# Optimization experiments

Measured on AMD Instinct MI355X. Metric: run time of the kernel, lower is better.

The kernel has to match this reference:

```python
import jax, jax.numpy as jnp
import numpy as np

B = 256      # graphs per batch
N_PER = 256  # nodes per graph
DEG = 16     # avg degree
F_IN = 128   # num_feats
H = 128      # nhid
C = 10       # num_classes
RATIO = 0.5
N = B * N_PER
E = B * N_PER * DEG
K1 = int(np.ceil(RATIO * N_PER))   # 128
K2 = int(np.ceil(RATIO * K1))      # 64
K3 = int(np.ceil(RATIO * K2))      # 32


def setup_inputs() -> dict:
    key = jax.random.key(0)
    ks = jax.random.split(key, 24)
    off = (jnp.arange(B, dtype=jnp.int32) * N_PER)[:, None]
    # random intra-graph edges (block-diagonal adjacency)
    src = (jax.random.randint(ks[0], (B, N_PER * DEG), 0, N_PER, dtype=jnp.int32) + off).reshape(-1)
    dst = (jax.random.randint(ks[1], (B, N_PER * DEG), 0, N_PER, dtype=jnp.int32) + off).reshape(-1)
    x = jax.random.normal(ks[2], (N, F_IN), jnp.float32)

    def glorot(k, fi, fo):
        s = jnp.sqrt(2.0 / (fi + fo)).astype(jnp.float32)
        return jax.random.normal(k, (fi, fo), jnp.float32) * s

    inp = dict(x=x, src=src, dst=dst)
    # GCN conv layers
    inp['W1'] = glorot(ks[3], F_IN, H); inp['b1'] = jnp.zeros((H,), jnp.float32)
    inp['W2'] = glorot(ks[4], H, H);    inp['b2'] = jnp.zeros((H,), jnp.float32)
    inp['W3'] = glorot(ks[5], H, H);    inp['b3'] = jnp.zeros((H,), jnp.float32)
    # SAGPool score layers (GCNConv(nhid, 1))
    inp['Ws1'] = glorot(ks[6], H, 1); inp['bs1'] = jnp.zeros((1,), jnp.float32)
    inp['Ws2'] = glorot(ks[7], H, 1); inp['bs2'] = jnp.zeros((1,), jnp.float32)
    inp['Ws3'] = glorot(ks[8], H, 1); inp['bs3'] = jnp.zeros((1,), jnp.float32)
    # MLP head
    inp['Wl1'] = glorot(ks[9], 2 * H, H);      inp['bl1'] = jnp.zeros((H,), jnp.float32)
    inp['Wl2'] = glorot(ks[10], H, H // 2);    inp['bl2'] = jnp.zeros((H // 2,), jnp.float32)
    inp['Wl3'] = glorot(ks[11], H // 2, C);    inp['bl3'] = jnp.zeros((C,), jnp.float32)
    return inp


def _gcn(x, W, b, src, dst, mask):
    # PyG GCNConv: add self-loops, sym-normalize by deg^-1/2, aggregate x@W.
    # `mask` marks surviving nodes; edges with a dropped endpoint are inactive,
    # which is equivalent to PyG's filter_adj subgraph relabeling.
    emf = (mask[src] & mask[dst]).astype(x.dtype)           # [E]
    deg = jax.ops.segment_sum(emf, dst, num_segments=N) + mask.astype(x.dtype)  # +1 self loop
    dinv = jnp.where(deg > 0, jax.lax.rsqrt(deg), 0.0)
    h = x @ W                                                # [N, out]
    w = emf * dinv[src] * dinv[dst]                          # [E]
    agg = jax.ops.segment_sum(h[src] * w[:, None], dst, num_segments=N)
    agg = agg + h * (dinv * dinv * mask.astype(x.dtype))[:, None]  # self-loop term
    return agg + b


def _sagpool(x, Ws, bs, src, dst, mask, k):
    # score = GCNConv(in,1)(x); keep top-k per graph; x = x[perm]*tanh(score[perm])
    score = _gcn(x, Ws, bs, src, dst, mask)[:, 0]            # [N]
    s = jnp.where(mask, score, -jnp.inf).reshape(B, N_PER)
    idx = jax.lax.top_k(s, k)[1]                             # [B, k]
    nm = jnp.zeros((B, N_PER), bool).at[jnp.arange(B)[:, None], idx].set(True).reshape(-1)
    x = x * jnp.tanh(score)[:, None] * nm[:, None].astype(x.dtype)
    return x, nm


def _readout(x, mask, count):
    # global_max_pool || global_mean_pool over surviving nodes of each graph
    xb = x.reshape(B, N_PER, H)
    mb = mask.reshape(B, N_PER)[:, :, None]
    mx = jnp.max(jnp.where(mb, xb, -jnp.inf), axis=1)
    mn = jnp.sum(xb * mb.astype(x.dtype), axis=1) / jnp.asarray(count, x.dtype)
    return jnp.concatenate([mx, mn], axis=1)                 # [B, 2H]


def reference(x, src, dst, W1, b1, W2, b2, W3, b3, Ws1, bs1, Ws2, bs2, Ws3, bs3,
              Wl1, bl1, Wl2, bl2, Wl3, bl3):
    m0 = jnp.ones((N,), bool)
    h = jax.nn.relu(_gcn(x, W1, b1, src, dst, m0))
    h, m1 = _sagpool(h, Ws1, bs1, src, dst, m0, K1)
    r1 = _readout(h, m1, K1)
    h = jax.nn.relu(_gcn(h, W2, b2, src, dst, m1))
    h, m2 = _sagpool(h, Ws2, bs2, src, dst, m1, K2)
    r2 = _readout(h, m2, K2)
    h = jax.nn.relu(_gcn(h, W3, b3, src, dst, m2))
    h, m3 = _sagpool(h, Ws3, bs3, src, dst, m2, K3)
    r3 = _readout(h, m3, K3)
    z = r1 + r2 + r3                                         # [B, 2H]
    z = jax.nn.relu(z @ Wl1 + bl1)
    # dropout skipped (eval mode / training=False)
    z = jax.nn.relu(z @ Wl2 + bl2)
    return jax.nn.log_softmax(jax.nn.relu(z @ Wl3 + bl3), axis=-1)
```

## Files before the change

### kernel.cpp

```cpp
#include <hip/hip_runtime.h>
#include <math.h>

#define NGRAPH 256
#define NPG 256
#define HF 128
#define EPG 4096
#define EPG2 4352
#define FSTR 132
#define PSTR 136

typedef __attribute__((ext_vector_type(8))) short bf16x8;
typedef __attribute__((ext_vector_type(4))) float f32x4;

template<int N> struct IC { static constexpr int value = N; };
template<bool B> struct BC { static constexpr bool value = B; };

static __device__ __forceinline__ unsigned bcu(float f){ return __builtin_bit_cast(unsigned, f); }
static __device__ __forceinline__ float bcf(unsigned u){ return __builtin_bit_cast(float, u); }
static __device__ __forceinline__ unsigned rtn16(float f){
  unsigned u = bcu(f);
  return (u + 0x7FFFu + ((u >> 16) & 1u)) >> 16;
}

__global__ __launch_bounds__(256) void prep_wt(const float* __restrict__ W1,
                                               const float* __restrict__ W2,
                                               const float* __restrict__ W3,
                                               short* __restrict__ Wt) {
  int idx = blockIdx.x * 256 + threadIdx.x;
  int L = idx >> 14, r = idx & 16383;
  int k = r >> 7, n = r & 127;
  const float* W = (L == 0) ? W1 : (L == 1) ? W2 : W3;
  float w = W[k*128 + n];
  unsigned hi = rtn16(w);
  float lo = w - bcf(hi << 16);
  short* Whi = Wt + (size_t)L * 2 * 16384;
  short* Wlo = Whi + 16384;
  Whi[n*128 + k] = (short)hi;
  Wlo[n*128 + k] = (short)(bcu(lo) >> 16);
}

#define BSTEP(OK, OI, KKc, Jc) do { \
  bool iLess = ((tid & (Jc)) == 0); \
  bool descR = ((tid & (KKc)) == 0); \
  bool myFirst = (kf > (OK)) || (kf == (OK) && ki < (OI)); \
  bool keep = (iLess == descR) ? myFirst : !myFirst; \
  if (!keep) { kf = (OK); ki = (OI); } \
} while (0)

#define WAVE0_SCAN() do { \
  if (wid == 0) { \
    int b4 = lane*4; \
    int c0=cntA[b4+0], c1=cntA[b4+1], c2=cntA[b4+2], c3=cntA[b4+3]; \
    int tot = c0+c1+c2+c3; \
    int run = tot; \
    _Pragma("unroll") \
    for (int off=1; off<64; off<<=1) { \
      int u = __shfl_up(run, off); \
      run += (lane >= off) ? u : 0; \
    } \
    int st = run - tot; \
    rloc[b4+0]=(unsigned short)st; \
    rloc[b4+1]=(unsigned short)(st+c0); \
    rloc[b4+2]=(unsigned short)(st+c0+c1); \
    rloc[b4+3]=(unsigned short)(st+c0+c1+c2); \
    curA[b4+0]=st; curA[b4+1]=st+c0; curA[b4+2]=st+c0+c1; curA[b4+3]=st+c0+c1+c2; \
    if (lane == 63) rloc[NPG] = (unsigned short)run; \
  } \
} while (0)

__global__ __launch_bounds__(1024, 4)
void fused_net(
    const float* __restrict__ x,
    const int* __restrict__ srcI, const int* __restrict__ dstI,
    const short* __restrict__ WtAll,
    const float* __restrict__ b1, const float* __restrict__ Ws1, const float* __restrict__ bs1,
    const float* __restrict__ b2, const float* __restrict__ Ws2, const float* __restrict__ bs2,
    const float* __restrict__ b3, const float* __restrict__ Ws3, const float* __restrict__ bs3,
    const float* __restrict__ Wl1, const float* __restrict__ bl1,
    const float* __restrict__ Wl2, const float* __restrict__ bl2,
    const float* __restrict__ Wl3, const float* __restrict__ bl3,
    float* __restrict__ out)
{
  __shared__ __align__(16) short hpair[2][NPG*PSTR];
  __shared__ unsigned char colS[EPG2 + 8];
  __shared__ unsigned short rloc[NPG+2];
  __shared__ unsigned selM[8];
  __shared__ float dinv[NPG];
  __shared__ __align__(16) float bvec[HF];
  __shared__ __align__(16) float wsv[HF];
  __shared__ float score[NPG];
  __shared__ float tscale[NPG];
  __shared__ float skey[NPG];
  __shared__ int   sidx[NPG];
  __shared__ unsigned char rank8[NPG];
  __shared__ unsigned char lut[NPG];
  __shared__ __align__(16) float red[1024];
  __shared__ float zacc[2*HF];

  float* tbufF = (float*)&hpair[0][0];
  short* hp0 = &hpair[0][0];
  short* hp1 = &hpair[1][0];
  int* cntA = (int*)skey;
  int* curA = sidx;

  int tid = threadIdx.x;
  int g = blockIdx.x;
  size_t nbase = (size_t)g * NPG;
  int lane = tid & 63, wid = tid >> 6;

  const float4* X4 = (const float4*)(x + nbase*HF);
  #pragma unroll
  for (int i = 0; i < 8; ++i) {
    int f4 = tid + i*1024;
    int r = f4 >> 5, kq = f4 & 31;
    float4 val = X4[f4];
    unsigned rx = rtn16(val.x), ry = rtn16(val.y), rz = rtn16(val.z), rw = rtn16(val.w);
    uint2 ph; ph.x = rx | (ry << 16); ph.y = rz | (rw << 16);
    float lx = val.x - bcf(rx << 16), ly = val.y - bcf(ry << 16);
    float lz = val.z - bcf(rz << 16), lw = val.w - bcf(rw << 16);
    uint2 pl; pl.x = (bcu(lx) >> 16) | (bcu(ly) & 0xFFFF0000u);
    pl.y = (bcu(lz) >> 16) | (bcu(lw) & 0xFFFF0000u);
    *(uint2*)&hp0[r*PSTR + kq*4] = ph;
    *(uint2*)&hp1[r*PSTR + kq*4] = pl;
  }

  int nb = g * NPG;
  int dloc[4], sloc[4];
  #pragma unroll
  for (int it = 0; it < 4; ++it) {
    int e = g*EPG + tid + it*1024;
    dloc[it] = dstI[e] - nb;
    sloc[it] = srcI[e] - nb;
  }

  if (tid < NPG) { cntA[tid] = 1; lut[tid] = (unsigned char)tid; }
  __syncthreads();
  #pragma unroll
  for (int it = 0; it < 4; ++it) atomicAdd(&cntA[dloc[it]], 1);
  __syncthreads();
  WAVE0_SCAN();
  __syncthreads();
  #pragma unroll
  for (int it = 0; it < 4; ++it) {
    int slot = atomicAdd(&curA[dloc[it]], 1);
    colS[slot] = (unsigned char)sloc[it];
  }
  if (tid < NPG) colS[rloc[tid+1] - 1] = (unsigned char)tid;

  auto run_layer = [&](auto nrc, auto kc, auto firstc, auto packc,
                       const short* Whi, const short* Wlo,
                       const float* bias, const float* Wsc, const float* bscp) {
    constexpr int NR = decltype(nrc)::value;
    constexpr int K  = decltype(kc)::value;
    constexpr bool FIRST = decltype(firstc)::value;
    constexpr bool PACK  = decltype(packc)::value;
    constexpr int TPN = 1024 / NR;
    constexpr int NI  = 32 / TPN;
    constexpr int SH  = (TPN == 4) ? 2 : ((TPN == 8) ? 3 : 4);
    int v = tid >> SH, q = tid & (TPN - 1);
    int cb0 = 4 * q;

    __syncthreads();

    if (tid < HF) { bvec[tid] = bias[tid]; wsv[tid] = Wsc[tid]; }
    if (tid < NR) dinv[tid] = 1.0f / sqrtf((float)((int)rloc[tid+1] - (int)rloc[tid]));

    {
      int rg = wid & 7, cg = wid >> 3;
      bool act = (rg * 32 < NR);
      int lr = lane & 15, lk8 = (lane >> 4) * 8;
      f32x4 tacc[2][4] = {};
      if (act) {
        #pragma unroll
        for (int kc2 = 0; kc2 < 4; ++kc2) {
          int k0 = kc2*32 + lk8;
          bf16x8 ah[2], al[2];
          #pragma unroll
          for (int rt = 0; rt < 2; ++rt) {
            int row = rg*32 + rt*16 + lr;
            ah[rt] = *(const bf16x8*)&hp0[row*PSTR + k0];
            al[rt] = *(const bf16x8*)&hp1[row*PSTR + k0];
          }
          #pragma unroll
          for (int ct = 0; ct < 4; ++ct) {
            int n = cg*64 + ct*16 + lr;
            bf16x8 bh = *(const bf16x8*)&Whi[n*HF + k0];
            bf16x8 bl = *(const bf16x8*)&Wlo[n*HF + k0];
            #pragma unroll
            for (int rt = 0; rt < 2; ++rt) {
              tacc[rt][ct] = __builtin_amdgcn_mfma_f32_16x16x32_bf16(ah[rt], bh, tacc[rt][ct], 0, 0, 0);
              tacc[rt][ct] = __builtin_amdgcn_mfma_f32_16x16x32_bf16(al[rt], bh, tacc[rt][ct], 0, 0, 0);
              tacc[rt][ct] = __builtin_amdgcn_mfma_f32_16x16x32_bf16(ah[rt], bl, tacc[rt][ct], 0, 0, 0);
            }
          }
        }
      }
      __syncthreads();
      if (act) {
        #pragma unroll
        for (int rt = 0; rt < 2; ++rt) {
          int row0 = rg*32 + rt*16 + (lane >> 4)*4;
          float d0 = dinv[row0+0], d1 = dinv[row0+1], d2 = dinv[row0+2], d3 = dinv[row0+3];
          #pragma unroll
          for (int ct = 0; ct < 4; ++ct) {
            int c = cg*64 + ct*16 + (lane & 15);
            tbufF[(row0+0)*FSTR + c] = tacc[rt][ct][0] * d0;
            tbufF[(row0+1)*FSTR + c] = tacc[rt][ct][1] * d1;
            tbufF[(row0+2)*FSTR + c] = tacc[rt][ct][2] * d2;
            tbufF[(row0+3)*FSTR + c] = tacc[rt][ct][3] * d3;
          }
        }
      }
    }
    __syncthreads();

    float4 hv[NI];
    {
      float4 acc[NI];
      #pragma unroll
      for (int j = 0; j < NI; ++j) { acc[j].x = acc[j].y = acc[j].z = acc[j].w = 0.f; }
      int e0 = rloc[v], e1 = rloc[v+1];
      int e = e0;
      for (; e + 1 < e1; e += 2) {
        int s0 = colS[e], s1 = colS[e+1];
        const float* g0 = &tbufF[s0*FSTR + cb0];
        const float* g1 = &tbufF[s1*FSTR + cb0];
        #pragma unroll
        for (int j = 0; j < NI; ++j) {
          float4 t0 = *(const float4*)&g0[j*4*TPN];
          float4 t1 = *(const float4*)&g1[j*4*TPN];
          acc[j].x += t0.x + t1.x; acc[j].y += t0.y + t1.y;
          acc[j].z += t0.z + t1.z; acc[j].w += t0.w + t1.w;
        }
      }
      if (e < e1) {
        const float* g0 = &tbufF[(int)colS[e]*FSTR + cb0];
        #pragma unroll
        for (int j = 0; j < NI; ++j) {
          float4 t0 = *(const float4*)&g0[j*4*TPN];
          acc[j].x += t0.x; acc[j].y += t0.y; acc[j].z += t0.z; acc[j].w += t0.w;
        }
      }
      float dv = dinv[v];
      float p = 0.f;
      #pragma unroll
      for (int j = 0; j < NI; ++j) {
        int ci = cb0 + j*4*TPN;
        float4 bv = *(const float4*)&bvec[ci];
        float4 wv = *(const float4*)&wsv[ci];
        float4 a;
        a.x = fmaxf(fmaf(dv, acc[j].x, bv.x), 0.f);
        a.y = fmaxf(fmaf(dv, acc[j].y, bv.y), 0.f);
        a.z = fmaxf(fmaf(dv, acc[j].z, bv.z), 0.f);
        a.w = fmaxf(fmaf(dv, acc[j].w, bv.w), 0.f);
        hv[j] = a;
        p += a.x*wv.x + a.y*wv.y + a.z*wv.z + a.w*wv.w;
      }
      red[tid] = p;
    }
    __syncthreads();
    if (tid < NR) {
      float s4 = 0.f;
      #pragma unroll
      for (int t = 0; t < TPN/4; ++t) {
        float4 qd = *(const float4*)&red[tid*TPN + 4*t];
        s4 += (qd.x + qd.y) + (qd.z + qd.w);
      }
      tscale[tid] = s4 * dinv[tid];
    }
    __syncthreads();
    if (tid < NR) {
      int e0 = rloc[tid], e1 = rloc[tid+1];
      float sa = 0.f;
      for (int e = e0; e < e1; ++e) sa += tscale[colS[e]];
      score[tid] = dinv[tid] * sa + bscp[0];
    }
    __syncthreads();

    float kf = -INFINITY; int ki = tid;
    if (tid < NR) {
      kf = score[tid];
      for (int kk = 2; kk <= 64; kk <<= 1)
        for (int j = kk >> 1; j > 0; j >>= 1) {
          float ok = __shfl_xor(kf, j);
          int   oi = __shfl_xor(ki, j);
          BSTEP(ok, oi, kk, j);
        }
    } else if (tid < NR + 8) selM[tid - NR] = 0u;

    if constexpr (NR == 256) {
      if (tid < NR) { skey[tid] = kf; sidx[tid] = ki; }
      __syncthreads();
      if (tid < NR) {
        int l = tid ^ 64; float ok = skey[l]; int oi = sidx[l];
        BSTEP(ok, oi, 128, 64);
        for (int j = 32; j > 0; j >>= 1) {
          float sk = __shfl_xor(kf, j); int si = __shfl_xor(ki, j);
          BSTEP(sk, si, 128, j);
        }
      }
      __syncthreads();
      if (tid < NR) { skey[tid] = kf; sidx[tid] = ki; }
      __syncthreads();
      if (tid < NR) {
        int l = tid ^ 128; float ok = skey[l]; int oi = sidx[l];
        BSTEP(ok, oi, 256, 128);
      }
      __syncthreads();
      if (tid < NR) { skey[tid] = kf; sidx[tid] = ki; }
      __syncthreads();
      if (tid < NR) {
        int l = tid ^ 64; float ok = skey[l]; int oi = sidx[l];
        BSTEP(ok, oi, 256, 64);
        for (int j = 32; j > 0; j >>= 1) {
          float sk = __shfl_xor(kf, j); int si = __shfl_xor(ki, j);
          BSTEP(sk, si, 256, j);
        }
      }
    } else if constexpr (NR == 128) {
      if (tid < NR) { skey[tid] = kf; sidx[tid] = ki; }
      __syncthreads();
      if (tid < NR) {
        int l = tid ^ 64; float ok = skey[l]; int oi = sidx[l];
        BSTEP(ok, oi, 128, 64);
        for (int j = 32; j > 0; j >>= 1) {
          float sk = __shfl_xor(kf, j); int si = __shfl_xor(ki, j);
          BSTEP(sk, si, 128, j);
        }
      }
    }
    if constexpr (NR == 64) __syncthreads();
    if constexpr (NR != 64 && NR != 256) __syncthreads();
    if (tid < K) atomicOr(&selM[ki >> 5], 1u << (ki & 31));
    __syncthreads();

    if (tid < NR) {
      unsigned wsel = selM[tid >> 5];
      bool sel = (wsel >> (tid & 31)) & 1;
      int r = __popc(wsel & ((1u << (tid & 31)) - 1u));
      for (int w = 0; w < (tid >> 5); ++w) r += __popc(selM[w]);
      rank8[tid] = sel ? (unsigned char)r : (unsigned char)0xFF;
      tscale[tid] = sel ? tanhf(score[tid]) : 0.f;
    }
    __syncthreads();
    if (tid < NPG) {
      int lv = lut[tid];
      lut[tid] = (lv < NR) ? rank8[lv] : (unsigned char)0xFF;
    }

    int rk = rank8[v];
    {
      float ts = tscale[v];
      if (rk != 0xFF) {
        #pragma unroll
        for (int j = 0; j < NI; ++j) {
          hv[j].x *= ts; hv[j].y *= ts; hv[j].z *= ts; hv[j].w *= ts;
          *(float4*)&tbufF[rk*FSTR + cb0 + j*4*TPN] = hv[j];
        }
      }
    }
    __syncthreads();

    {
      constexpr int RPG = K / 8;
      int f = tid & 127, vg = tid >> 7;
      float mx = -INFINITY, sm = 0.f;
      #pragma unroll
      for (int vr = 0; vr < RPG; ++vr) {
        float val = tbufF[(vg*RPG + vr)*FSTR + f];
        mx = fmaxf(mx, val); sm += val;
      }
      red[vg*HF + f] = mx;
      __syncthreads();
      if (tid < HF) {
        float zm = red[tid];
        #pragma unroll
        for (int q2 = 1; q2 < 8; ++q2) zm = fmaxf(zm, red[q2*HF + tid]);
        if (FIRST) zacc[tid] = zm; else zacc[tid] += zm;
      }
      __syncthreads();
      red[vg*HF + f] = sm;
      __syncthreads();
      if (tid < HF) {
        float zs = red[tid];
        #pragma unroll
        for (int q2 = 1; q2 < 8; ++q2) zs += red[q2*HF + tid];
        float mn = zs / (float)K;
        if (FIRST) zacc[HF + tid] = mn; else zacc[HF + tid] += mn;
      }
      __syncthreads();
    }

    if constexpr (PACK) {
      if (rk != 0xFF) {
        #pragma unroll
        for (int j = 0; j < NI; ++j) {
          int ci = cb0 + j*4*TPN;
          float4 val = hv[j];
          unsigned rx = rtn16(val.x), ry = rtn16(val.y), rz = rtn16(val.z), rw = rtn16(val.w);
          uint2 ph; ph.x = rx | (ry << 16); ph.y = rz | (rw << 16);
          float lx = val.x - bcf(rx << 16), ly = val.y - bcf(ry << 16);
          float lz = val.z - bcf(rz << 16), lw = val.w - bcf(rw << 16);
          uint2 pl; pl.x = (bcu(lx) >> 16) | (bcu(ly) & 0xFFFF0000u);
          pl.y = (bcu(lz) >> 16) | (bcu(lw) & 0xFFFF0000u);
          *(uint2*)&hp0[rk*PSTR + ci] = ph;
          *(uint2*)&hp1[rk*PSTR + ci] = pl;
        }
      }

      if (tid < K) cntA[tid] = 1; else if (tid < NPG) cntA[tid] = 0;
      __syncthreads();
      #pragma unroll
      for (int it = 0; it < 4; ++it) {
        int d2 = lut[dloc[it]], s2 = lut[sloc[it]];
        if (d2 < K && s2 < K) atomicAdd(&cntA[d2], 1);
      }
      __syncthreads();
      WAVE0_SCAN();
      __syncthreads();
      #pragma unroll
      for (int it = 0; it < 4; ++it) {
        int d2 = lut[dloc[it]], s2 = lut[sloc[it]];
        if (d2 < K && s2 < K) {
          int slot = atomicAdd(&curA[d2], 1);
          colS[slot] = (unsigned char)s2;
        }
      }
      if (tid < K) colS[rloc[tid+1] - 1] = (unsigned char)tid;
    }
  };

  run_layer(IC<256>{}, IC<128>{}, BC<true>{},  BC<true>{},
            WtAll,         WtAll + 16384, b1, Ws1, bs1);
  run_layer(IC<128>{}, IC<64>{},  BC<false>{}, BC<true>{},
            WtAll + 32768, WtAll + 49152, b2, Ws2, bs2);
  run_layer(IC<64>{},  IC<32>{},  BC<false>{}, BC<false>{},
            WtAll + 65536, WtAll + 81920, b3, Ws3, bs3);

  __syncthreads();

  {
    int o = tid & 127, kg = tid >> 7;
    float p = 0.f;
    int k0 = kg*32;
    for (int k = k0; k < k0+32; ++k) p += zacc[k]*Wl1[k*HF + o];
    red[kg*HF + o] = p;
    __syncthreads();
    if (tid < HF) {
      float a = bl1[tid];
      #pragma unroll
      for (int q2 = 0; q2 < 8; ++q2) a += red[q2*HF + tid];
      score[tid] = fmaxf(a, 0.f);
    }
    __syncthreads();
    if (tid < 512) {
      int o2 = tid & 63, kg2 = tid >> 6;
      float p2 = 0.f;
      int k0b = kg2*16;
      for (int k = k0b; k < k0b+16; ++k) p2 += score[k]*Wl2[k*64 + o2];
      red[kg2*64 + o2] = p2;
    }
    __syncthreads();
    if (tid < 64) {
      float a = bl2[tid];
      #pragma unroll
      for (int q2 = 0; q2 < 8; ++q2) a += red[q2*64 + tid];
      tscale[tid] = fmaxf(a, 0.f);
    }
    __syncthreads();
    if (tid < 10) {
      float a = bl3[tid];
      for (int k = 0; k < 64; ++k) a += tscale[k]*Wl3[k*10 + tid];
      dinv[tid] = fmaxf(a, 0.f);
    }
    __syncthreads();
    if (tid == 0) {
      float m = dinv[0];
      for (int i = 1; i < 10; ++i) m = fmaxf(m, dinv[i]);
      float s = 0.f;
      for (int i = 0; i < 10; ++i) s += expf(dinv[i] - m);
      red[0] = m; red[1] = logf(s);
    }
    __syncthreads();
    if (tid < 10) out[(size_t)g*10 + tid] = dinv[tid] - red[0] - red[1];
  }
}

extern "C" void kernel_launch(void* const* d_in, const int* in_sizes, int n_in,
                              void* d_out, int out_size, void* d_ws, size_t ws_size,
                              hipStream_t stream) {
  const float* x   = (const float*)d_in[0];
  const int*  srcI = (const int*)d_in[1];
  const int*  dstI = (const int*)d_in[2];
  const float* W1  = (const float*)d_in[3];
  const float* b1  = (const float*)d_in[4];
  const float* W2  = (const float*)d_in[5];
  const float* b2  = (const float*)d_in[6];
  const float* W3  = (const float*)d_in[7];
  const float* b3  = (const float*)d_in[8];
  const float* Ws1 = (const float*)d_in[9];
  const float* bs1 = (const float*)d_in[10];
  const float* Ws2 = (const float*)d_in[11];
  const float* bs2 = (const float*)d_in[12];
  const float* Ws3 = (const float*)d_in[13];
  const float* bs3 = (const float*)d_in[14];
  const float* Wl1 = (const float*)d_in[15];
  const float* bl1 = (const float*)d_in[16];
  const float* Wl2 = (const float*)d_in[17];
  const float* bl2 = (const float*)d_in[18];
  const float* Wl3 = (const float*)d_in[19];
  const float* bl3 = (const float*)d_in[20];
  float* out = (float*)d_out;

  short* WtAll = (short*)d_ws;

  prep_wt<<<192, 256, 0, stream>>>(W1, W2, W3, WtAll);
  fused_net<<<NGRAPH, 1024, 0, stream>>>(x, srcI, dstI, WtAll,
                                         b1, Ws1, bs1, b2, Ws2, bs2, b3, Ws3, bs3,
                                         Wl1, bl1, Wl2, bl2, Wl3, bl3, out);
}
```

Before: 93.69 us.

## Rebalance MFMA tiling across all waves, prefetch neighbor indices, merge readout reductions

```diff
diff --git a/kernel.cpp b/kernel.cpp
--- a/kernel.cpp
+++ b/kernel.cpp
@@ -95,6 +95,7 @@
   __shared__ unsigned char rank8[NPG];
   __shared__ unsigned char lut[NPG];
   __shared__ __align__(16) float red[1024];
+  __shared__ __align__(16) float red2[1024];
   __shared__ float zacc[2*HF];
 
   float* tbufF = (float*)&hpair[0][0];
@@ -157,6 +158,7 @@
     constexpr int TPN = 1024 / NR;
     constexpr int NI  = 32 / TPN;
     constexpr int SH  = (TPN == 4) ? 2 : ((TPN == 8) ? 3 : 4);
+    constexpr int RT  = NR / 64;
     int v = tid >> SH, q = tid & (TPN - 1);
     int cb0 = 4 * q;
 
@@ -166,49 +168,44 @@
     if (tid < NR) dinv[tid] = 1.0f / sqrtf((float)((int)rloc[tid+1] - (int)rloc[tid]));
 
     {
-      int rg = wid & 7, cg = wid >> 3;
-      bool act = (rg * 32 < NR);
+      int rg = wid & 3, cg = wid >> 2;
       int lr = lane & 15, lk8 = (lane >> 4) * 8;
-      f32x4 tacc[2][4] = {};
-      if (act) {
-        #pragma unroll
-        for (int kc2 = 0; kc2 < 4; ++kc2) {
-          int k0 = kc2*32 + lk8;
-          bf16x8 ah[2], al[2];
+      f32x4 tacc[RT][2] = {};
+      #pragma unroll
+      for (int kc2 = 0; kc2 < 4; ++kc2) {
+        int k0 = kc2*32 + lk8;
+        bf16x8 ah[RT], al[RT];
+        #pragma unroll
+        for (int rt = 0; rt < RT; ++rt) {
+          int row = rg*(NR/4) + rt*16 + lr;
+          ah[rt] = *(const bf16x8*)&hp0[row*PSTR + k0];
+          al[rt] = *(const bf16x8*)&hp1[row*PSTR + k0];
+        }
+        #pragma unroll
+        for (int ct = 0; ct < 2; ++ct) {
+          int n = cg*32 + ct*16 + lr;
+          bf16x8 bh = *(const bf16x8*)&Whi[n*HF + k0];
+          bf16x8 bl = *(const bf16x8*)&Wlo[n*HF + k0];
           #pragma unroll
-          for (int rt = 0; rt < 2; ++rt) {
-            int row = rg*32 + rt*16 + lr;
-            ah[rt] = *(const bf16x8*)&hp0[row*PSTR + k0];
-            al[rt] = *(const bf16x8*)&hp1[row*PSTR + k0];
+          for (int rt = 0; rt < RT; ++rt) {
+            tacc[rt][ct] = __builtin_amdgcn_mfma_f32_16x16x32_bf16(ah[rt], bh, tacc[rt][ct], 0, 0, 0);
+            tacc[rt][ct] = __builtin_amdgcn_mfma_f32_16x16x32_bf16(al[rt], bh, tacc[rt][ct], 0, 0, 0);
+            tacc[rt][ct] = __builtin_amdgcn_mfma_f32_16x16x32_bf16(ah[rt], bl, tacc[rt][ct], 0, 0, 0);
           }
-          #pragma unroll
-          for (int ct = 0; ct < 4; ++ct) {
-            int n = cg*64 + ct*16 + lr;
-            bf16x8 bh = *(const bf16x8*)&Whi[n*HF + k0];
-            bf16x8 bl = *(const bf16x8*)&Wlo[n*HF + k0];
-            #pragma unroll
-            for (int rt = 0; rt < 2; ++rt) {
-              tacc[rt][ct] = __builtin_amdgcn_mfma_f32_16x16x32_bf16(ah[rt], bh, tacc[rt][ct], 0, 0, 0);
-              tacc[rt][ct] = __builtin_amdgcn_mfma_f32_16x16x32_bf16(al[rt], bh, tacc[rt][ct], 0, 0, 0);
-              tacc[rt][ct] = __builtin_amdgcn_mfma_f32_16x16x32_bf16(ah[rt], bl, tacc[rt][ct], 0, 0, 0);
-            }
-          }
-        }
-      }
-      __syncthreads();
-      if (act) {
-        #pragma unroll
-        for (int rt = 0; rt < 2; ++rt) {
-          int row0 = rg*32 + rt*16 + (lane >> 4)*4;
-          float d0 = dinv[row0+0], d1 = dinv[row0+1], d2 = dinv[row0+2], d3 = dinv[row0+3];
-          #pragma unroll
-          for (int ct = 0; ct < 4; ++ct) {
-            int c = cg*64 + ct*16 + (lane & 15);
-            tbufF[(row0+0)*FSTR + c] = tacc[rt][ct][0] * d0;
-            tbufF[(row0+1)*FSTR + c] = tacc[rt][ct][1] * d1;
-            tbufF[(row0+2)*FSTR + c] = tacc[rt][ct][2] * d2;
-            tbufF[(row0+3)*FSTR + c] = tacc[rt][ct][3] * d3;
-          }
+        }
+      }
+      __syncthreads();
+      #pragma unroll
+      for (int rt = 0; rt < RT; ++rt) {
+        int row0 = rg*(NR/4) + rt*16 + (lane >> 4)*4;
+        float d0 = dinv[row0+0], d1 = dinv[row0+1], d2 = dinv[row0+2], d3 = dinv[row0+3];
+        #pragma unroll
+        for (int ct = 0; ct < 2; ++ct) {
+          int c = cg*32 + ct*16 + (lane & 15);
+          tbufF[(row0+0)*FSTR + c] = tacc[rt][ct][0] * d0;
+          tbufF[(row0+1)*FSTR + c] = tacc[rt][ct][1] * d1;
+          tbufF[(row0+2)*FSTR + c] = tacc[rt][ct][2] * d2;
+          tbufF[(row0+3)*FSTR + c] = tacc[rt][ct][3] * d3;
         }
       }
     }
@@ -220,9 +217,11 @@
       #pragma unroll
       for (int j = 0; j < NI; ++j) { acc[j].x = acc[j].y = acc[j].z = acc[j].w = 0.f; }
       int e0 = rloc[v], e1 = rloc[v+1];
+      int sA = colS[e0], sB = colS[e0+1], sC = colS[e0+2], sD = colS[e0+3];
       int e = e0;
       for (; e + 1 < e1; e += 2) {
-        int s0 = colS[e], s1 = colS[e+1];
+        int s0 = sA, s1 = sB;
+        sA = sC; sB = sD; sC = colS[e+4]; sD = colS[e+5];
         const float* g0 = &tbufF[s0*FSTR + cb0];
         const float* g1 = &tbufF[s1*FSTR + cb0];
         #pragma unroll
@@ -234,7 +233,7 @@
         }
       }
       if (e < e1) {
-        const float* g0 = &tbufF[(int)colS[e]*FSTR + cb0];
+        const float* g0 = &tbufF[sA*FSTR + cb0];
         #pragma unroll
         for (int j = 0; j < NI; ++j) {
           float4 t0 = *(const float4*)&g0[j*4*TPN];
@@ -272,7 +271,11 @@
     if (tid < NR) {
       int e0 = rloc[tid], e1 = rloc[tid+1];
       float sa = 0.f;
-      for (int e = e0; e < e1; ++e) sa += tscale[colS[e]];
+      int sA = colS[e0], sB = colS[e0+1], sC = colS[e0+2], sD = colS[e0+3];
+      for (int e = e0; e < e1; ++e) {
+        int s = sA; sA = sB; sB = sC; sC = sD; sD = colS[e+4];
+        sa += tscale[s];
+      }
       score[tid] = dinv[tid] * sa + bscp[0];
     }
     __syncthreads();
@@ -371,22 +374,19 @@
         mx = fmaxf(mx, val); sm += val;
       }
       red[vg*HF + f] = mx;
+      red2[vg*HF + f] = sm;
       __syncthreads();
       if (tid < HF) {
         float zm = red[tid];
-        #pragma unroll
-        for (int q2 = 1; q2 < 8; ++q2) zm = fmaxf(zm, red[q2*HF + tid]);
-        if (FIRST) zacc[tid] = zm; else zacc[tid] += zm;
-      }
-      __syncthreads();
-      red[vg*HF + f] = sm;
-      __syncthreads();
-      if (tid < HF) {
-        float zs = red[tid];
-        #pragma unroll
-        for (int q2 = 1; q2 < 8; ++q2) zs += red[q2*HF + tid];
+        float zs = red2[tid];
+        #pragma unroll
+        for (int q2 = 1; q2 < 8; ++q2) {
+          zm = fmaxf(zm, red[q2*HF + tid]);
+          zs += red2[q2*HF + tid];
+        }
         float mn = zs / (float)K;
-        if (FIRST) zacc[HF + tid] = mn; else zacc[HF + tid] += mn;
+        if (FIRST) { zacc[tid] = zm; zacc[HF + tid] = mn; }
+        else       { zacc[tid] += zm; zacc[HF + tid] += mn; }
       }
       __syncthreads();
     }
```

Measured after the change: 84.07 us. -10.3%, faster.
